# Kernel optimization log

Hardware: AMD Instinct MI355X
Metric: run time of the kernel (lower is better)

Reference implementation:

```python
import jax, jax.numpy as jnp
import numpy as np
import math

T, C, S = 16, 4, 256
DT = 0.05
JITTER = 1e-05
IDENTITY_MIX = 0.05
MIN_BLOCK_SCALE = 0.01
CLIP = 1e4
MAX_TRIES = 8


def _sym(m):
    return 0.5 * (m + jnp.swapaxes(m, -1, -2))


def _san_m(m):
    return _sym(jnp.clip(jnp.nan_to_num(m, nan=0.0, posinf=CLIP, neginf=-CLIP), -CLIP, CLIP))


def _san_v(v):
    return jnp.clip(jnp.nan_to_num(v, nan=0.0, posinf=CLIP, neginf=-CLIP), -CLIP, CLIP)


def _stable_inv_logdet(mat, base_jitter):
    # mat: [..., 2, 2] symmetric. Vectorized closed-form version of the per-block
    # Cholesky retry loop: for a 2x2 SPD matrix [[a,b],[b,c]], cholesky succeeds
    # iff a > 0 and det = a*c - b^2 > 0; inverse = adj/det; logdet = log(det).
    eye = jnp.eye(2, dtype=mat.dtype)
    cand = _san_m(mat)
    diag = jnp.diagonal(cand, axis1=-2, axis2=-1)                    # [..., 2]
    diag_scale = jnp.maximum(jnp.mean(jnp.abs(diag), axis=-1), 1.0)  # [...]
    j0 = max(base_jitter, 1e-6)
    jitters = j0 * (10.0 ** jnp.arange(MAX_TRIES, dtype=mat.dtype))  # [K]
    jit_b = jitters.reshape((MAX_TRIES,) + (1,) * diag_scale.ndim) * diag_scale[None]  # [K, ...]
    rep = _san_m(cand[None] + jit_b[..., None, None] * eye)          # [K, ..., 2, 2]
    a, b, c = rep[..., 0, 0], rep[..., 0, 1], rep[..., 1, 1]
    det = a * c - b * b
    ok = (a > 0) & (det > 0)
    idx = jnp.argmax(ok, axis=0)                                     # first successful jitter level
    any_ok = jnp.any(ok, axis=0)
    gather = lambda x: jnp.take_along_axis(x, idx[None], axis=0)[0]
    a0, b0, c0 = gather(a), gather(b), gather(c)
    det0 = jnp.where(any_ok, a0 * c0 - b0 * b0, 1.0)
    rep0 = jnp.take_along_axis(rep, idx[None, ..., None, None], axis=0)[0]
    inv0 = jnp.stack([jnp.stack([c0, -b0], -1), jnp.stack([-b0, a0], -1)], -2) / det0[..., None, None]
    inv0 = _san_m(inv0)
    logdet0 = jnp.nan_to_num(jnp.log(det0), nan=0.0, posinf=20.0, neginf=-20.0)
    # fallback: all tries failed -> diagonal repair
    jit_f = j0 * (10.0 ** MAX_TRIES)
    sd = jnp.nan_to_num(diag, nan=1.0, posinf=CLIP, neginf=1.0)
    sd = jnp.maximum(jnp.abs(sd), (jit_f * diag_scale)[..., None] + 1e-4)
    rep_f = _san_m(sd[..., None] * eye + (jit_f * diag_scale)[..., None, None] * eye)
    dg_f = jnp.maximum(jnp.diagonal(rep_f, axis1=-2, axis2=-1), 1e-6)
    inv_f = _san_m((1.0 / dg_f)[..., None] * eye)
    logdet_f = jnp.nan_to_num(jnp.sum(jnp.log(dg_f), -1), nan=0.0, posinf=20.0, neginf=-20.0)
    m = any_ok[..., None, None]
    repaired = jnp.where(m, rep0, rep_f)
    inverse = jnp.where(m, inv0, inv_f)
    log_det = jnp.where(any_ok, logdet0, logdet_f)
    return repaired, inverse, log_det


def setup_inputs() -> dict:
    key = jax.random.key(0)
    k1, k2, k3 = jax.random.split(key, 3)
    means = jax.random.normal(k1, (T, C, 2), dtype=jnp.float32)
    covariances = jax.random.normal(k2, (T, C, 2, 2), dtype=jnp.float32)
    site_coords = jax.random.normal(k3, (S, 2), dtype=jnp.float32) * 3.0
    block_scale_raw = jnp.full((C, C), 0.25, dtype=jnp.float32).at[jnp.arange(C), jnp.arange(C)].set(1.0)
    identity_mix_logit = jnp.asarray(math.log(IDENTITY_MIX / (1.0 - IDENTITY_MIX)), dtype=jnp.float32)
    return {"means": means, "covariances": covariances, "site_coords": site_coords,
            "block_scale_raw": block_scale_raw, "identity_mix_logit": identity_mix_logit}


def reference(means, covariances, site_coords, block_scale_raw, identity_mix_logit):
    means = _san_v(means)                                              # [T, C, 2]
    covs = _san_m(covariances)                                         # [T, C, 2, 2]
    lags = _san_v(site_coords[:, None, :] - site_coords[None, :, :])   # [S, S, 2]
    scales = jax.nn.softplus(block_scale_raw) + MIN_BLOCK_SCALE        # [C, C]
    mix = jax.nn.sigmoid(identity_mix_logit)
    eye2 = jnp.eye(2, dtype=means.dtype)
    drift = _san_v(DT * (means[:, :, None, :] - means[:, None, :, :])) # [T, C, C, 2]
    disp = eye2 + 2.0 * DT ** 2 * (covs[:, :, None] + covs[:, None, :])
    disp = _san_m(disp + JITTER * eye2)
    disp, inv, logdet = _stable_inv_logdet(disp, JITTER)               # [T,C,C,2,2], [T,C,C]
    centered = _san_v(lags[None, None, None] - drift[:, :, :, None, None, :])  # [T,C,C,S,S,2]
    quad = jnp.einsum('tijabk,tijkl,tijabl->tijab', centered, inv, centered)
    quad = jnp.clip(jnp.nan_to_num(quad, nan=0.0, posinf=60.0, neginf=0.0), 0.0, 60.0)
    expo = jnp.clip(-0.5 * logdet[..., None, None] - quad, -60.0, 20.0)
    block = jnp.nan_to_num(scales[None, :, :, None, None] * jnp.exp(expo), nan=0.0, posinf=0.0, neginf=0.0)
    t, c, s = means.shape[0], means.shape[1], site_coords.shape[0]
    # blocks laid out row-major in (component, site): index (i*S+a, j*S+b)
    K = jnp.transpose(block, (0, 1, 3, 2, 4)).reshape(t, c * s, c * s)
    tr = jnp.nan_to_num(K / jnp.maximum(K.sum(-1, keepdims=True), JITTER), nan=0.0, posinf=0.0, neginf=0.0)
    tr = tr / jnp.maximum(tr.sum(-1, keepdims=True), JITTER)
    ident = jnp.eye(c * s, dtype=tr.dtype)
    tr = (1.0 - mix) * tr + mix * ident
    tr = jnp.nan_to_num(tr, nan=0.0, posinf=0.0, neginf=0.0)
    tr = tr / jnp.maximum(tr.sum(-1, keepdims=True), JITTER)
    return tr, drift, disp, scales, mix
```

## Files before the change

### kernel.cpp

```cpp
#include <hip/hip_runtime.h>
#include <math.h>

#define T_ 16
#define C_ 4
#define S_ 256
static constexpr float DT      = 0.05f;
static constexpr float JITTER  = 1e-5f;
static constexpr float CLIPV   = 1e4f;

typedef float f32x4 __attribute__((ext_vector_type(4)));

static constexpr int TR_SIZE     = T_ * (C_ * S_) * (C_ * S_);
static constexpr int DRIFT_OFF   = TR_SIZE;
static constexpr int DISP_OFF    = DRIFT_OFF + T_ * C_ * C_ * 2;
static constexpr int SCALES_OFF  = DISP_OFF + T_ * C_ * C_ * 4;
static constexpr int MIX_OFF     = SCALES_OFF + C_ * C_;

static constexpr int WS_REC = 8;
static constexpr int WS_MIX = T_ * C_ * C_ * WS_REC;

__device__ __forceinline__ float sanv(float x) {
    if (isnan(x)) return 0.f;
    return fminf(fmaxf(x, -CLIPV), CLIPV);
}

__global__ __launch_bounds__(256)
void prep_kernel(const float* __restrict__ means,
                 const float* __restrict__ covs,
                 const float* __restrict__ bsr,
                 const float* __restrict__ mixlogit,
                 float* __restrict__ out,
                 float* __restrict__ ws) {
    int tid = threadIdx.x;
    if (tid >= T_ * C_ * C_) return;
    int t = tid >> 4;
    int i = (tid >> 2) & 3;
    int j = tid & 3;
    int bl = tid;

    float mix_ = sanv(means[(t * C_ + i) * 2 + 0]);
    float miy  = sanv(means[(t * C_ + i) * 2 + 1]);
    float mjx  = sanv(means[(t * C_ + j) * 2 + 0]);
    float mjy  = sanv(means[(t * C_ + j) * 2 + 1]);
    float dx = sanv(DT * (mix_ - mjx));
    float dy = sanv(DT * (miy - mjy));
    out[DRIFT_OFF + bl * 2 + 0] = dx;
    out[DRIFT_OFF + bl * 2 + 1] = dy;

    const float* ci = covs + (t * C_ + i) * 4;
    const float* cj = covs + (t * C_ + j) * 4;
    float ci00 = sanv(ci[0]), ci01 = 0.5f * (sanv(ci[1]) + sanv(ci[2])), ci11 = sanv(ci[3]);
    float cj00 = sanv(cj[0]), cj01 = 0.5f * (sanv(cj[1]) + sanv(cj[2])), cj11 = sanv(cj[3]);

    const float k2 = 2.0f * DT * DT;
    float a = sanv(1.0f + k2 * (ci00 + cj00) + JITTER);
    float b = sanv(        k2 * (ci01 + cj01));
    float c = sanv(1.0f + k2 * (ci11 + cj11) + JITTER);

    float ds = fmaxf(0.5f * (fabsf(a) + fabsf(c)), 1.0f);
    float ra = 0.f, rb = 0.f, rc = 0.f, det0 = 1.f;
    bool found = false;
    float jit = 1e-5f;
    #pragma unroll
    for (int k = 0; k < 8; ++k) {
        float ja = sanv(a + jit * ds);
        float jb = sanv(b);
        float jc = sanv(c + jit * ds);
        float det = ja * jc - jb * jb;
        if (!found && ja > 0.f && det > 0.f) {
            found = true; ra = ja; rb = jb; rc = jc; det0 = det;
        }
        jit *= 10.f;
    }

    float i00, i01, i11, ld, o00, o01, o11;
    if (found) {
        i00 = sanv(rc / det0);
        i01 = sanv(-rb / det0);
        i11 = sanv(ra / det0);
        ld = logf(det0);
        if (isnan(ld)) ld = 0.f;
        else if (isinf(ld)) ld = (ld > 0.f) ? 20.f : -20.f;
        o00 = ra; o01 = rb; o11 = rc;
    } else {
        float jf = 1e3f;
        float sd0 = fmaxf(fabsf(a), jf * ds + 1e-4f);
        float sd1 = fmaxf(fabsf(c), jf * ds + 1e-4f);
        o00 = sanv(sd0 + jf * ds); o11 = sanv(sd1 + jf * ds); o01 = 0.f;
        float dg0 = fmaxf(o00, 1e-6f), dg1 = fmaxf(o11, 1e-6f);
        i00 = sanv(1.f / dg0); i11 = sanv(1.f / dg1); i01 = 0.f;
        ld = logf(dg0) + logf(dg1);
        if (isnan(ld)) ld = 0.f;
        else if (isinf(ld)) ld = (ld > 0.f) ? 20.f : -20.f;
    }
    out[DISP_OFF + bl * 4 + 0] = o00;
    out[DISP_OFF + bl * 4 + 1] = o01;
    out[DISP_OFF + bl * 4 + 2] = o01;
    out[DISP_OFF + bl * 4 + 3] = o11;

    float x = bsr[i * 4 + j];
    float sc = fmaxf(x, 0.f) + log1pf(expf(-fabsf(x))) + 0.01f;
    if (t == 0) out[SCALES_OFF + i * 4 + j] = sc;

    float* w = ws + bl * WS_REC;
    w[0] = i00; w[1] = i01; w[2] = i11; w[3] = -0.5f * ld;
    w[4] = dx;  w[5] = dy;  w[6] = sc;  w[7] = 0.f;

    if (tid == 0) {
        float lg = mixlogit[0];
        float mx = 1.f / (1.f + expf(-lg));
        out[MIX_OFF] = mx;
        ws[WS_MIX]   = mx;
    }
}

__global__ __launch_bounds__(256)
void row_kernel(const float* __restrict__ site,
                const float* __restrict__ ws,
                float* __restrict__ tr) {
    __shared__ float sdata[4];
    int r = blockIdx.x;
    int t = r >> 10;
    int i = (r >> 8) & 3;
    int a = r & 255;
    int tid = threadIdx.x;
    int lane = tid & 63;
    int wid = __builtin_amdgcn_readfirstlane(tid >> 6);

    const f32x4* s4 = (const f32x4*)site;
    f32x4 p0 = s4[2 * lane];
    f32x4 p1 = s4[2 * lane + 1];
    float2 sa = ((const float2*)site)[a];
    float mx = ws[WS_MIX];

    const float* w = ws + ((t * C_ + i) * C_ + wid) * WS_REC;
    float i00 = w[0], i01 = w[1], i11 = w[2], h = w[3];
    float dx = w[4],  dy = w[5],  sc = w[6];
    float ox = sa.x - dx, oy = sa.y - dy;

    float bx[4] = {p0.x, p0.z, p1.x, p1.z};
    float by[4] = {p0.y, p0.w, p1.y, p1.w};

    float v[4];
    #pragma unroll
    for (int k = 0; k < 4; ++k) {
        float cx = ox - bx[k], cy = oy - by[k];
        float u = i00 * cx + i01 * cy;
        float z = i01 * cx + i11 * cy;
        float q = cx * u + cy * z;
        q = fminf(fmaxf(q, 0.f), 60.f);
        float e = fminf(fmaxf(h - q, -60.f), 20.f);
        v[k] = sc * __expf(e);
    }

    float local = (v[0] + v[1]) + (v[2] + v[3]);
    #pragma unroll
    for (int off = 32; off > 0; off >>= 1) local += __shfl_down(local, off, 64);
    if (lane == 0) sdata[wid] = local;
    __syncthreads();
    float s1 = sdata[0] + sdata[1] + sdata[2] + sdata[3];

    float d1 = fmaxf(s1, JITTER);
    float r1 = __builtin_amdgcn_rcpf(d1);
    float s2 = s1 * r1;
    float d2 = fmaxf(s2, JITTER);
    float r2 = __builtin_amdgcn_rcpf(d2);
    float sum_t2 = s2 * r2;
    float omx = 1.f - mx;
    float s3 = omx * sum_t2 + mx;
    float d3 = fmaxf(s3, JITTER);
    float r3 = __builtin_amdgcn_rcpf(d3);
    float scale = omx * r1 * r2 * r3;
    float diag  = mx * r3;

    f32x4 o;
    o.x = v[0] * scale; o.y = v[1] * scale;
    o.z = v[2] * scale; o.w = v[3] * scale;
    if (wid == i && lane == (a >> 2)) {
        int sl = a & 3;
        if      (sl == 0) o.x += diag;
        else if (sl == 1) o.y += diag;
        else if (sl == 2) o.z += diag;
        else              o.w += diag;
    }

    size_t base = ((size_t)t << 20) + (size_t)(i * S_ + a) * 1024;
    __builtin_nontemporal_store(o, (f32x4*)(tr + base) + tid);
}

extern "C" void kernel_launch(void* const* d_in, const int* in_sizes, int n_in,
                              void* d_out, int out_size, void* d_ws, size_t ws_size,
                              hipStream_t stream) {
    const float* means    = (const float*)d_in[0];
    const float* covs     = (const float*)d_in[1];
    const float* site     = (const float*)d_in[2];
    const float* bsr      = (const float*)d_in[3];
    const float* mixlogit = (const float*)d_in[4];
    float* out = (float*)d_out;
    float* ws  = (float*)d_ws;

    prep_kernel<<<1, 256, 0, stream>>>(means, covs, bsr, mixlogit, out, ws);
    row_kernel<<<T_ * C_ * S_, 256, 0, stream>>>(site, ws, out);
}
```

Baseline: 93.83 us.

## Assign one output row per wavefront instead of per block

```diff
diff --git a/kernel.cpp b/kernel.cpp
--- a/kernel.cpp
+++ b/kernel.cpp
@@ -118,14 +118,12 @@
 void row_kernel(const float* __restrict__ site,
                 const float* __restrict__ ws,
                 float* __restrict__ tr) {
-    __shared__ float sdata[4];
-    int r = blockIdx.x;
+    int tid  = threadIdx.x;
+    int lane = tid & 63;
+    int r = __builtin_amdgcn_readfirstlane((blockIdx.x << 2) | (tid >> 6));
     int t = r >> 10;
     int i = (r >> 8) & 3;
     int a = r & 255;
-    int tid = threadIdx.x;
-    int lane = tid & 63;
-    int wid = __builtin_amdgcn_readfirstlane(tid >> 6);
 
     const f32x4* s4 = (const f32x4*)site;
     f32x4 p0 = s4[2 * lane];
@@ -133,32 +131,34 @@
     float2 sa = ((const float2*)site)[a];
     float mx = ws[WS_MIX];
 
-    const float* w = ws + ((t * C_ + i) * C_ + wid) * WS_REC;
-    float i00 = w[0], i01 = w[1], i11 = w[2], h = w[3];
-    float dx = w[4],  dy = w[5],  sc = w[6];
-    float ox = sa.x - dx, oy = sa.y - dy;
-
     float bx[4] = {p0.x, p0.z, p1.x, p1.z};
     float by[4] = {p0.y, p0.w, p1.y, p1.w};
 
-    float v[4];
+    float v[4][4];
+    float local = 0.f;
     #pragma unroll
     for (int k = 0; k < 4; ++k) {
-        float cx = ox - bx[k], cy = oy - by[k];
-        float u = i00 * cx + i01 * cy;
-        float z = i01 * cx + i11 * cy;
-        float q = cx * u + cy * z;
-        q = fminf(fmaxf(q, 0.f), 60.f);
-        float e = fminf(fmaxf(h - q, -60.f), 20.f);
-        v[k] = sc * __expf(e);
-    }
-
-    float local = (v[0] + v[1]) + (v[2] + v[3]);
-    #pragma unroll
-    for (int off = 32; off > 0; off >>= 1) local += __shfl_down(local, off, 64);
-    if (lane == 0) sdata[wid] = local;
-    __syncthreads();
-    float s1 = sdata[0] + sdata[1] + sdata[2] + sdata[3];
+        const float* w = ws + ((t * C_ + i) * C_ + k) * WS_REC;
+        float i00 = w[0], i01 = w[1], i11 = w[2], h = w[3];
+        float dx = w[4],  dy = w[5],  sc = w[6];
+        float ox = sa.x - dx, oy = sa.y - dy;
+        #pragma unroll
+        for (int s = 0; s < 4; ++s) {
+            float cx = ox - bx[s], cy = oy - by[s];
+            float u = i00 * cx + i01 * cy;
+            float z = i01 * cx + i11 * cy;
+            float q = cx * u + cy * z;
+            q = fminf(fmaxf(q, 0.f), 60.f);
+            float e = fminf(fmaxf(h - q, -60.f), 20.f);
+            float val = sc * __expf(e);
+            v[k][s] = val;
+            local += val;
+        }
+    }
+
+    #pragma unroll
+    for (int m = 1; m < 64; m <<= 1) local += __shfl_xor(local, m, 64);
+    float s1 = local;
 
     float d1 = fmaxf(s1, JITTER);
     float r1 = __builtin_amdgcn_rcpf(d1);
@@ -173,19 +173,22 @@
     float scale = omx * r1 * r2 * r3;
     float diag  = mx * r3;
 
-    f32x4 o;
-    o.x = v[0] * scale; o.y = v[1] * scale;
-    o.z = v[2] * scale; o.w = v[3] * scale;
-    if (wid == i && lane == (a >> 2)) {
-        int sl = a & 3;
-        if      (sl == 0) o.x += diag;
-        else if (sl == 1) o.y += diag;
-        else if (sl == 2) o.z += diag;
-        else              o.w += diag;
-    }
-
     size_t base = ((size_t)t << 20) + (size_t)(i * S_ + a) * 1024;
-    __builtin_nontemporal_store(o, (f32x4*)(tr + base) + tid);
+    f32x4* dst = (f32x4*)(tr + base);
+    #pragma unroll
+    for (int k = 0; k < 4; ++k) {
+        f32x4 o;
+        o.x = v[k][0] * scale; o.y = v[k][1] * scale;
+        o.z = v[k][2] * scale; o.w = v[k][3] * scale;
+        if (k == i && lane == (a >> 2)) {
+            int sl = a & 3;
+            if      (sl == 0) o.x += diag;
+            else if (sl == 1) o.y += diag;
+            else if (sl == 2) o.z += diag;
+            else              o.w += diag;
+        }
+        __builtin_nontemporal_store(o, dst + (k << 6) + lane);
+    }
 }
 
 extern "C" void kernel_launch(void* const* d_in, const int* in_sizes, int n_in,
@@ -200,5 +203,5 @@
     float* ws  = (float*)d_ws;
 
     prep_kernel<<<1, 256, 0, stream>>>(means, covs, bsr, mixlogit, out, ws);
-    row_kernel<<<T_ * C_ * S_, 256, 0, stream>>>(site, ws, out);
-}
+    row_kernel<<<(T_ * C_ * S_) / 4, 256, 0, stream>>>(site, ws, out);
+}
```

Result: faster. 90.19 us (-3.9%).
